# Kernel tuning notes

Hardware: AMD Instinct MI355X
Metric: run time of the kernel (lower is better)

## Reference

```python
import jax, jax.numpy as jnp
import numpy as np

B, N, D, DG = 32, 2048, 512, 1024


def layernorm(x, g, b, eps=1e-5):
    m = jnp.mean(x, axis=-1, keepdims=True)
    v = jnp.mean((x - m) ** 2, axis=-1, keepdims=True)
    return (x - m) * jax.lax.rsqrt(v + eps) * g + b


def simple_rms_norm(x, eps=1e-6):
    # parameter-free RMSNorm used inside Hgru1d
    return x * jax.lax.rsqrt(jnp.mean(x * x, axis=-1, keepdims=True) + eps)


def linear_recurrence(lam, u, reverse):
    # h_t = lam_t * h_{t-1} + u_t along axis=1, via associative scan
    def comb(c1, c2):
        a1, b1 = c1
        a2, b2 = c2
        return a1 * a2, a2 * b1 + b2
    return jax.lax.associative_scan(comb, (lam, u), axis=1, reverse=reverse)[1]


def hgru1d(x, lower_bound, Wi, bi, Wf, bf, Wg, bg, Wo, bo):
    # HGRN-style gated recurrence, bidirectional (causal=False, shared params)
    i = jax.nn.silu(x @ Wi + bi)                       # candidate input  [b,n,d]
    f = jax.nn.sigmoid(x @ Wf + bf)                    # forget gate      [b,n,d]
    lam = lower_bound + (1.0 - lower_bound) * f        # lower-bounded decay
    u = (1.0 - lam) * i
    h = linear_recurrence(lam, u, False) + linear_recurrence(lam, u, True)
    h = simple_rms_norm(h)
    g = jax.nn.sigmoid(x @ Wg + bg)                    # output gate
    return (h * g) @ Wo + bo


def glu(x, W1, b1, W2, b2, W3, b3):
    return (jax.nn.silu(x @ W1 + b1) * (x @ W2 + b2)) @ W3 + b3


def setup_inputs() -> dict:
    key = jax.random.key(0)
    ks = jax.random.split(key, 16)
    s = 0.02
    return {
        "x": jax.random.normal(ks[0], (B, N, D), dtype=jnp.float32),
        "lower_bound": 0,
        "Wi": jax.random.normal(ks[1], (D, D), jnp.float32) * s,
        "bi": jnp.zeros((D,), jnp.float32),
        "Wf": jax.random.normal(ks[2], (D, D), jnp.float32) * s,
        "bf": jnp.zeros((D,), jnp.float32),
        "Wg": jax.random.normal(ks[3], (D, D), jnp.float32) * s,
        "bg": jnp.zeros((D,), jnp.float32),
        "Wo": jax.random.normal(ks[4], (D, D), jnp.float32) * s,
        "bo": jnp.zeros((D,), jnp.float32),
        "tn_g": jnp.ones((D,), jnp.float32),
        "tn_b": jnp.zeros((D,), jnp.float32),
        "fn_g": jnp.ones((D,), jnp.float32),
        "fn_b": jnp.zeros((D,), jnp.float32),
        "W1": jax.random.normal(ks[5], (D, DG), jnp.float32) * s,
        "b1": jnp.zeros((DG,), jnp.float32),
        "W2": jax.random.normal(ks[6], (D, DG), jnp.float32) * s,
        "b2": jnp.zeros((DG,), jnp.float32),
        "W3": jax.random.normal(ks[7], (DG, D), jnp.float32) * s,
        "b3": jnp.zeros((D,), jnp.float32),
    }


def reference(x, lower_bound, Wi, bi, Wf, bf, Wg, bg, Wo, bo,
              tn_g, tn_b, fn_g, fn_b, W1, b1, W2, b2, W3, b3):
    lb = jnp.float32(lower_bound)
    # post-norm residual block
    x = x + layernorm(hgru1d(x, lb, Wi, bi, Wf, bf, Wg, bg, Wo, bo), tn_g, tn_b)
    x = x + layernorm(glu(x, W1, b1, W2, b2, W3, b3), fn_g, fn_b)
    return x
```

## Files before the change

kernel.cpp:

```cpp
#include <hip/hip_runtime.h>
#include <hip/hip_bf16.h>

#define BB 32
#define NN 2048
#define DD 512
#define DGG 1024
#define CC 32
#define LLEN 64

typedef short bf16x8 __attribute__((ext_vector_type(8)));
typedef float f32x4  __attribute__((ext_vector_type(4)));

__device__ __forceinline__ unsigned short f2bf(float f){
    __hip_bfloat16 h = __float2bfloat16(f);
    return *reinterpret_cast<unsigned short*>(&h);
}
__device__ __forceinline__ float bf2f(unsigned short u){
    unsigned int x = ((unsigned int)u) << 16;
    return __uint_as_float(x);
}
__device__ __forceinline__ float sigm(float x){ return 1.0f/(1.0f + __expf(-x)); }

__global__ __launch_bounds__(256)
void wt_prep(const float* __restrict__ in, unsigned short* __restrict__ out,
             int K, int N)
{
    __shared__ float t[32][33];
    const int tid = threadIdx.x;
    const int r = tid >> 3;
    const int c = (tid & 7) << 2;
    const int n0 = blockIdx.x * 32;
    const int k0 = blockIdx.y * 32;
    float4 v = *(const float4*)(in + (size_t)(k0 + r) * N + n0 + c);
    t[r][c] = v.x; t[r][c+1] = v.y; t[r][c+2] = v.z; t[r][c+3] = v.w;
    __syncthreads();
    ushort4 o;
    o.x = f2bf(t[c+0][r]); o.y = f2bf(t[c+1][r]);
    o.z = f2bf(t[c+2][r]); o.w = f2bf(t[c+3][r]);
    *(ushort4*)(out + (size_t)(n0 + r) * K + k0 + c) = o;
}

template<int MODE, int NB, bool ABF16>
__global__ __launch_bounds__(256)
void gemm_kernel(const void* __restrict__ Ap,
                 const unsigned short* __restrict__ Bt0,
                 const unsigned short* __restrict__ Bt1,
                 const unsigned short* __restrict__ Bt2,
                 const float* __restrict__ bias0, const float* __restrict__ bias1,
                 const float* __restrict__ bias2,
                 unsigned short* __restrict__ out0, unsigned short* __restrict__ out1,
                 unsigned short* __restrict__ out2,
                 const int* __restrict__ lbp, int K, int Nn)
{
    __shared__ unsigned short As[64][40];
    __shared__ unsigned short Bs[NB][64][40];

    const int tid  = threadIdx.x;
    const int m0   = blockIdx.y * 64;
    const int n0   = blockIdx.x * 64;
    const int lane = tid & 63;
    const int wave = tid >> 6;
    const int wr   = (wave >> 1) * 32;
    const int wc   = (wave & 1) * 32;
    const int lm   = lane & 15;
    const int quad = lane >> 4;

    f32x4 acc[NB][2][2];
    const f32x4 zero = {0.f, 0.f, 0.f, 0.f};
    #pragma unroll
    for (int a = 0; a < NB; ++a)
        for (int i = 0; i < 2; ++i)
            for (int j = 0; j < 2; ++j) acc[a][i][j] = zero;

    const float* Af = (const float*)Ap;
    const unsigned short* Ab = (const unsigned short*)Ap;
    const unsigned short* Bmats[3] = {Bt0, Bt1, Bt2};

    const int srow = tid >> 2;
    const int sc8  = (tid & 3) << 3;

    for (int k0 = 0; k0 < K; k0 += 32) {
        if (!ABF16) {
            #pragma unroll
            for (int it = 0; it < 2; ++it) {
                int cidx = tid + it * 256;
                int row  = cidx >> 3;
                int c4   = (cidx & 7) << 2;
                float4 v = *(const float4*)(Af + (size_t)(m0 + row) * K + k0 + c4);
                ushort4 o;
                o.x = f2bf(v.x); o.y = f2bf(v.y); o.z = f2bf(v.z); o.w = f2bf(v.w);
                *(ushort4*)&As[row][c4] = o;
            }
        } else {
            bf16x8 v = *(const bf16x8*)(Ab + (size_t)(m0 + srow) * K + k0 + sc8);
            *(bf16x8*)&As[srow][sc8] = v;
        }
        #pragma unroll
        for (int mat = 0; mat < NB; ++mat) {
            bf16x8 v = *(const bf16x8*)(Bmats[mat] + (size_t)(n0 + srow) * K + k0 + sc8);
            *(bf16x8*)&Bs[mat][srow][sc8] = v;
        }
        __syncthreads();

        bf16x8 a0 = *(const bf16x8*)&As[wr + lm][quad * 8];
        bf16x8 a1 = *(const bf16x8*)&As[wr + 16 + lm][quad * 8];
        #pragma unroll
        for (int mat = 0; mat < NB; ++mat) {
            #pragma unroll
            for (int ni = 0; ni < 2; ++ni) {
                bf16x8 b = *(const bf16x8*)&Bs[mat][wc + ni * 16 + lm][quad * 8];
                acc[mat][0][ni] = __builtin_amdgcn_mfma_f32_16x16x32_bf16(a0, b, acc[mat][0][ni], 0, 0, 0);
                acc[mat][1][ni] = __builtin_amdgcn_mfma_f32_16x16x32_bf16(a1, b, acc[mat][1][ni], 0, 0, 0);
            }
        }
        __syncthreads();
    }

    float lbv = 0.f;
    if constexpr (MODE == 1) lbv = (float)(*lbp);

    #pragma unroll
    for (int mi = 0; mi < 2; ++mi) {
        #pragma unroll
        for (int ni = 0; ni < 2; ++ni) {
            #pragma unroll
            for (int r = 0; r < 4; ++r) {
                int row = m0 + wr + mi * 16 + quad * 4 + r;
                int col = n0 + wc + ni * 16 + lm;
                size_t oidx = (size_t)row * Nn + col;
                if constexpr (MODE == 0) {
                    out0[oidx] = f2bf(acc[0][mi][ni][r] + bias0[col]);
                } else if constexpr (MODE == 1) {
                    float iv = acc[0][mi][ni][r] + bias0[col]; iv = iv * sigm(iv);
                    float fv = sigm(acc[1][mi][ni][r] + bias1[col]);
                    float gv = sigm(acc[2][mi][ni][r] + bias2[col]);
                    float lamv = lbv + (1.f - lbv) * fv;
                    float uv = (1.f - lamv) * iv;
                    out0[oidx] = f2bf(lamv);
                    out1[oidx] = f2bf(uv);
                    out2[oidx] = f2bf(gv);
                } else {
                    float s = acc[0][mi][ni][r] + bias0[col]; s = s * sigm(s);
                    float t = acc[1][mi][ni][r] + bias1[col];
                    out0[oidx] = f2bf(s * t);
                }
            }
        }
    }
}

__global__ __launch_bounds__(512)
void scan_agg(const unsigned short* __restrict__ lam, const unsigned short* __restrict__ u,
              float* __restrict__ Aarr, float* __restrict__ Vf, float* __restrict__ Vr)
{
    int bc = blockIdx.x;
    int b = bc >> 5, c = bc & 31;
    int d = threadIdx.x;
    size_t base = ((size_t)b * NN + c * LLEN) * DD + d;
    float A = 1.f, vf = 0.f, vr = 0.f;
    for (int t = 0; t < LLEN; ++t) {
        float lv = bf2f(lam[base + (size_t)t * DD]);
        float uv = bf2f(u[base + (size_t)t * DD]);
        vf = lv * vf + uv;
        vr += uv * A;
        A *= lv;
    }
    size_t o = (size_t)bc * DD + d;
    Aarr[o] = A; Vf[o] = vf; Vr[o] = vr;
}

__global__ __launch_bounds__(256)
void scan_comb(const float* __restrict__ Aarr, const float* __restrict__ Vf,
               const float* __restrict__ Vr, float* __restrict__ cf, float* __restrict__ cr)
{
    int g = blockIdx.x * 256 + threadIdx.x;
    int b = g >> 9, d = g & 511;
    float S = 0.f;
    for (int c = 0; c < CC; ++c) {
        size_t o = (size_t)(b * CC + c) * DD + d;
        cf[o] = S;
        S = Vf[o] + Aarr[o] * S;
    }
    S = 0.f;
    for (int c = CC - 1; c >= 0; --c) {
        size_t o = (size_t)(b * CC + c) * DD + d;
        cr[o] = S;
        S = Vr[o] + Aarr[o] * S;
    }
}

__global__ __launch_bounds__(256)
void scan_final(const unsigned short* __restrict__ lam, const unsigned short* __restrict__ u,
                const float* __restrict__ cf, const float* __restrict__ cr,
                float* __restrict__ h)
{
    int bid = blockIdx.x;
    int dh = bid & 1, c = (bid >> 1) & 31, b = bid >> 6;
    int d = dh * 256 + threadIdx.x;
    size_t base = ((size_t)b * NN + c * LLEN) * DD + d;
    size_t co   = (size_t)(b * CC + c) * DD + d;

    float hbuf[LLEN];
    float hf = cf[co];
    #pragma unroll
    for (int t = 0; t < LLEN; ++t) {
        float lv = bf2f(lam[base + (size_t)t * DD]);
        float uv = bf2f(u[base + (size_t)t * DD]);
        hf = lv * hf + uv;
        hbuf[t] = hf;
    }
    float hr = cr[co];
    #pragma unroll
    for (int t = LLEN - 1; t >= 0; --t) {
        float lv = bf2f(lam[base + (size_t)t * DD]);
        float uv = bf2f(u[base + (size_t)t * DD]);
        hr = lv * hr + uv;
        h[base + (size_t)t * DD] = hbuf[t] + hr;
    }
}

__global__ __launch_bounds__(256)
void rms_mul(const float* __restrict__ h, const unsigned short* __restrict__ g,
             unsigned short* __restrict__ hg)
{
    int row = blockIdx.x;
    size_t base = (size_t)row * DD;
    int tid = threadIdx.x, col = tid * 2;
    float2 v = *(const float2*)&h[base + col];
    float ss = v.x * v.x + v.y * v.y;
    #pragma unroll
    for (int off = 32; off > 0; off >>= 1) ss += __shfl_down(ss, off);
    __shared__ float ps[4];
    __shared__ float scale_s;
    if ((tid & 63) == 0) ps[tid >> 6] = ss;
    __syncthreads();
    if (tid == 0) scale_s = rsqrtf((ps[0] + ps[1] + ps[2] + ps[3]) * (1.f / DD) + 1e-6f);
    __syncthreads();
    float sc = scale_s;
    ushort2 gv = *(const ushort2*)&g[base + col];
    ushort2 o;
    o.x = f2bf(v.x * sc * bf2f(gv.x));
    o.y = f2bf(v.y * sc * bf2f(gv.y));
    *(ushort2*)&hg[base + col] = o;
}

__global__ __launch_bounds__(256)
void add_ln(const float* __restrict__ xin, const unsigned short* __restrict__ y,
            const float* __restrict__ gam, const float* __restrict__ bet,
            float* __restrict__ out)
{
    int row = blockIdx.x;
    size_t base = (size_t)row * DD;
    int tid = threadIdx.x, col = tid * 2;
    ushort2 yv = *(const ushort2*)&y[base + col];
    float vx = bf2f(yv.x), vy = bf2f(yv.y);
    float s = vx + vy;
    float ss = vx * vx + vy * vy;
    #pragma unroll
    for (int off = 32; off > 0; off >>= 1) {
        s  += __shfl_down(s, off);
        ss += __shfl_down(ss, off);
    }
    __shared__ float ps[8];
    __shared__ float stats[2];
    if ((tid & 63) == 0) { ps[tid >> 6] = s; ps[4 + (tid >> 6)] = ss; }
    __syncthreads();
    if (tid == 0) {
        float st  = ps[0] + ps[1] + ps[2] + ps[3];
        float sst = ps[4] + ps[5] + ps[6] + ps[7];
        float mean = st * (1.f / DD);
        float var  = sst * (1.f / DD) - mean * mean;
        stats[0] = mean; stats[1] = rsqrtf(var + 1e-5f);
    }
    __syncthreads();
    float mean = stats[0], inv = stats[1];
    float2 xv = *(const float2*)&xin[base + col];
    float2 gv = *(const float2*)&gam[col];
    float2 bv = *(const float2*)&bet[col];
    float2 o;
    o.x = xv.x + (vx - mean) * inv * gv.x + bv.x;
    o.y = xv.y + (vy - mean) * inv * gv.y + bv.y;
    *(float2*)&out[base + col] = o;
}

extern "C" void kernel_launch(void* const* d_in, const int* in_sizes, int n_in,
                              void* d_out, int out_size, void* d_ws, size_t ws_size,
                              hipStream_t stream)
{
    const float* x   = (const float*)d_in[0];
    const int*   lb  = (const int*)d_in[1];
    const float* Wi  = (const float*)d_in[2];
    const float* bi  = (const float*)d_in[3];
    const float* Wf  = (const float*)d_in[4];
    const float* bfp = (const float*)d_in[5];
    const float* Wg  = (const float*)d_in[6];
    const float* bg  = (const float*)d_in[7];
    const float* Wo  = (const float*)d_in[8];
    const float* bo  = (const float*)d_in[9];
    const float* tng = (const float*)d_in[10];
    const float* tnb = (const float*)d_in[11];
    const float* fng = (const float*)d_in[12];
    const float* fnb = (const float*)d_in[13];
    const float* W1  = (const float*)d_in[14];
    const float* b1  = (const float*)d_in[15];
    const float* W2  = (const float*)d_in[16];
    const float* b2  = (const float*)d_in[17];
    const float* W3  = (const float*)d_in[18];
    const float* b3  = (const float*)d_in[19];

    unsigned short* wbase = (unsigned short*)d_ws;
    unsigned short* WiT = wbase;
    unsigned short* WfT = WiT + 262144;
    unsigned short* WgT = WfT + 262144;
    unsigned short* WoT = WgT + 262144;
    unsigned short* W1T = WoT + 262144;
    unsigned short* W2T = W1T + 524288;
    unsigned short* W3T = W2T + 524288;
    const size_t WTOT = 4 * 262144 + 3 * 524288;

    wt_prep<<<dim3(16, 16), 256, 0, stream>>>(Wi, WiT, 512, 512);
    wt_prep<<<dim3(16, 16), 256, 0, stream>>>(Wf, WfT, 512, 512);
    wt_prep<<<dim3(16, 16), 256, 0, stream>>>(Wg, WgT, 512, 512);
    wt_prep<<<dim3(16, 16), 256, 0, stream>>>(Wo, WoT, 512, 512);
    wt_prep<<<dim3(32, 16), 256, 0, stream>>>(W1, W1T, 512, 1024);
    wt_prep<<<dim3(32, 16), 256, 0, stream>>>(W2, W2T, 512, 1024);
    wt_prep<<<dim3(16, 32), 256, 0, stream>>>(W3, W3T, 1024, 512);

    const size_t perB = (size_t)3 * NN * DD * 2 + (size_t)5 * CC * DD * 4;
    int Bch = 32;
    while (Bch > 1 && WTOT * 2 + (size_t)Bch * perB > ws_size) Bch >>= 1;
    const int nch = BB / Bch;

    const size_t slabE = (size_t)Bch * NN * DD;

    for (int ch = 0; ch < nch; ++ch) {
        const size_t r0 = (size_t)ch * Bch * NN;
        const float* xc = x + r0 * DD;
        unsigned short* S0 = wbase + WTOT;
        unsigned short* S1 = S0 + slabE;
        unsigned short* S2 = S0 + 2 * slabE;
        float* small = (float*)(S0 + 3 * slabE);
        const size_t agg = (size_t)Bch * CC * DD;
        float* Aarr = small;
        float* VfP  = small + agg;
        float* VrP  = small + 2 * agg;
        float* cfP  = small + 3 * agg;
        float* crP  = small + 4 * agg;
        float* hout = (float*)d_out + r0 * DD;

        gemm_kernel<1, 3, false><<<dim3(DD / 64, Bch * NN / 64), 256, 0, stream>>>(
            xc, WiT, WfT, WgT, bi, bfp, bg, S0, S1, S2, lb, DD, DD);
        scan_agg<<<Bch * CC, 512, 0, stream>>>(S0, S1, Aarr, VfP, VrP);
        scan_comb<<<(Bch * DD) / 256, 256, 0, stream>>>(Aarr, VfP, VrP, cfP, crP);
        scan_final<<<Bch * CC * 2, 256, 0, stream>>>(S0, S1, cfP, crP, hout);
        rms_mul<<<Bch * NN, 256, 0, stream>>>(hout, S2, S2);
        gemm_kernel<0, 1, true><<<dim3(DD / 64, Bch * NN / 64), 256, 0, stream>>>(
            S2, WoT, nullptr, nullptr, bo, nullptr, nullptr, S0, nullptr, nullptr,
            nullptr, DD, DD);
        add_ln<<<Bch * NN, 256, 0, stream>>>(xc, S0, tng, tnb, hout);
        gemm_kernel<2, 2, false><<<dim3(DGG / 64, Bch * NN / 64), 256, 0, stream>>>(
            hout, W1T, W2T, nullptr, b1, b2, nullptr, S0, nullptr, nullptr, nullptr, DD, DGG);
        gemm_kernel<0, 1, true><<<dim3(DD / 64, Bch * NN / 64), 256, 0, stream>>>(
            S0, W3T, nullptr, nullptr, b3, nullptr, nullptr, S2, nullptr, nullptr,
            nullptr, DGG, DD);
        add_ln<<<Bch * NN, 256, 0, stream>>>(hout, S2, fng, fnb, hout);
    }
}
```

Before: 1.380 ms.

## Use 128x128 direct-to-LDS bf16 GEMM tiles and split fused multi-weight GEMMs

Replaces the 64x64 multi-matrix GEMM with a single-weight 128x128-tile GEMM that loads bf16 tiles into LDS via global_load_lds, giving each wave a 64x64 sub-tile with 16 MFMAs per k-step. Activations are pre-cast to bf16 by a new cast kernel, and add_ln also writes a bf16 copy so the GLU GEMMs read bf16 inputs. The fused three-gate and two-gate GEMMs are split into separate launches that pass intermediates through a staged buffer. The goal is more operand reuse per LDS load and less in-loop conversion, at the cost of extra launches, extra intermediate traffic and a larger workspace. The main loop still has no double buffering, and it is left uncertain whether direct LDS loads without padding cause bank conflicts.

```diff
diff --git a/kernel.cpp b/kernel.cpp
--- a/kernel.cpp
+++ b/kernel.cpp
@@ -20,6 +20,12 @@
     return __uint_as_float(x);
 }
 __device__ __forceinline__ float sigm(float x){ return 1.0f/(1.0f + __expf(-x)); }
+
+__device__ __forceinline__ void gl_lds16(const unsigned short* g, unsigned short* l){
+    __builtin_amdgcn_global_load_lds(
+        (const __attribute__((address_space(1))) unsigned int*)g,
+        (__attribute__((address_space(3))) unsigned int*)l, 16, 0, 0);
+}
 
 __global__ __launch_bounds__(256)
 void wt_prep(const float* __restrict__ in, unsigned short* __restrict__ out,
@@ -40,109 +46,105 @@
     *(ushort4*)(out + (size_t)(n0 + r) * K + k0 + c) = o;
 }
 
-template<int MODE, int NB, bool ABF16>
-__global__ __launch_bounds__(256)
-void gemm_kernel(const void* __restrict__ Ap,
-                 const unsigned short* __restrict__ Bt0,
-                 const unsigned short* __restrict__ Bt1,
-                 const unsigned short* __restrict__ Bt2,
-                 const float* __restrict__ bias0, const float* __restrict__ bias1,
-                 const float* __restrict__ bias2,
-                 unsigned short* __restrict__ out0, unsigned short* __restrict__ out1,
-                 unsigned short* __restrict__ out2,
-                 const int* __restrict__ lbp, int K, int Nn)
-{
-    __shared__ unsigned short As[64][40];
-    __shared__ unsigned short Bs[NB][64][40];
+__global__ __launch_bounds__(256)
+void cast_bf16(const float* __restrict__ in, unsigned short* __restrict__ out)
+{
+    size_t i = ((size_t)blockIdx.x * 256 + threadIdx.x) * 4;
+    float4 v = *(const float4*)(in + i);
+    ushort4 o;
+    o.x = f2bf(v.x); o.y = f2bf(v.y); o.z = f2bf(v.z); o.w = f2bf(v.w);
+    *(ushort4*)(out + i) = o;
+}
+
+template<int MODE>
+__global__ __launch_bounds__(256)
+void gemm128(const unsigned short* __restrict__ A,
+             const unsigned short* __restrict__ Bt,
+             const float* __restrict__ bias,
+             const unsigned short* __restrict__ staged,
+             unsigned short* __restrict__ out0,
+             unsigned short* __restrict__ out1,
+             const int* __restrict__ lbp, int K, int Nn)
+{
+    __shared__ unsigned short As[128 * 32];
+    __shared__ unsigned short Bs[128 * 32];
 
     const int tid  = threadIdx.x;
-    const int m0   = blockIdx.y * 64;
-    const int n0   = blockIdx.x * 64;
+    const int wave = tid >> 6;
     const int lane = tid & 63;
-    const int wave = tid >> 6;
-    const int wr   = (wave >> 1) * 32;
-    const int wc   = (wave & 1) * 32;
+    const int m0   = blockIdx.y * 128;
+    const int n0   = blockIdx.x * 128;
+    const int wr   = (wave >> 1) * 64;
+    const int wc   = (wave & 1) * 64;
     const int lm   = lane & 15;
     const int quad = lane >> 4;
 
-    f32x4 acc[NB][2][2];
+    f32x4 acc[4][4];
     const f32x4 zero = {0.f, 0.f, 0.f, 0.f};
     #pragma unroll
-    for (int a = 0; a < NB; ++a)
-        for (int i = 0; i < 2; ++i)
-            for (int j = 0; j < 2; ++j) acc[a][i][j] = zero;
-
-    const float* Af = (const float*)Ap;
-    const unsigned short* Ab = (const unsigned short*)Ap;
-    const unsigned short* Bmats[3] = {Bt0, Bt1, Bt2};
-
-    const int srow = tid >> 2;
-    const int sc8  = (tid & 3) << 3;
+    for (int i = 0; i < 4; ++i)
+        for (int j = 0; j < 4; ++j) acc[i][j] = zero;
+
+    const int srow = wave * 32 + (lane >> 2);
+    const int skof = (lane & 3) << 3;
+    const unsigned short* ga0 = A  + (size_t)(m0 + srow) * K + skof;
+    const unsigned short* ga1 = ga0 + (size_t)16 * K;
+    const unsigned short* gb0 = Bt + (size_t)(n0 + srow) * K + skof;
+    const unsigned short* gb1 = gb0 + (size_t)16 * K;
+    unsigned short* la0 = &As[(wave * 32) * 32];
+    unsigned short* la1 = &As[(wave * 32 + 16) * 32];
+    unsigned short* lb0 = &Bs[(wave * 32) * 32];
+    unsigned short* lb1 = &Bs[(wave * 32 + 16) * 32];
 
     for (int k0 = 0; k0 < K; k0 += 32) {
-        if (!ABF16) {
+        gl_lds16(ga0, la0); gl_lds16(ga1, la1);
+        gl_lds16(gb0, lb0); gl_lds16(gb1, lb1);
+        ga0 += 32; ga1 += 32; gb0 += 32; gb1 += 32;
+        __syncthreads();
+
+        bf16x8 a[4], b[4];
+        #pragma unroll
+        for (int mi = 0; mi < 4; ++mi)
+            a[mi] = *(const bf16x8*)&As[(wr + mi * 16 + lm) * 32 + quad * 8];
+        #pragma unroll
+        for (int ni = 0; ni < 4; ++ni)
+            b[ni] = *(const bf16x8*)&Bs[(wc + ni * 16 + lm) * 32 + quad * 8];
+        #pragma unroll
+        for (int mi = 0; mi < 4; ++mi)
             #pragma unroll
-            for (int it = 0; it < 2; ++it) {
-                int cidx = tid + it * 256;
-                int row  = cidx >> 3;
-                int c4   = (cidx & 7) << 2;
-                float4 v = *(const float4*)(Af + (size_t)(m0 + row) * K + k0 + c4);
-                ushort4 o;
-                o.x = f2bf(v.x); o.y = f2bf(v.y); o.z = f2bf(v.z); o.w = f2bf(v.w);
-                *(ushort4*)&As[row][c4] = o;
-            }
-        } else {
-            bf16x8 v = *(const bf16x8*)(Ab + (size_t)(m0 + srow) * K + k0 + sc8);
-            *(bf16x8*)&As[srow][sc8] = v;
-        }
+            for (int ni = 0; ni < 4; ++ni)
+                acc[mi][ni] = __builtin_amdgcn_mfma_f32_16x16x32_bf16(a[mi], b[ni], acc[mi][ni], 0, 0, 0);
+        __syncthreads();
+    }
+
+    float lbv = 0.f;
+    if constexpr (MODE == 3) lbv = (float)(*lbp);
+
+    #pragma unroll
+    for (int mi = 0; mi < 4; ++mi) {
         #pragma unroll
-        for (int mat = 0; mat < NB; ++mat) {
-            bf16x8 v = *(const bf16x8*)(Bmats[mat] + (size_t)(n0 + srow) * K + k0 + sc8);
-            *(bf16x8*)&Bs[mat][srow][sc8] = v;
-        }
-        __syncthreads();
-
-        bf16x8 a0 = *(const bf16x8*)&As[wr + lm][quad * 8];
-        bf16x8 a1 = *(const bf16x8*)&As[wr + 16 + lm][quad * 8];
-        #pragma unroll
-        for (int mat = 0; mat < NB; ++mat) {
-            #pragma unroll
-            for (int ni = 0; ni < 2; ++ni) {
-                bf16x8 b = *(const bf16x8*)&Bs[mat][wc + ni * 16 + lm][quad * 8];
-                acc[mat][0][ni] = __builtin_amdgcn_mfma_f32_16x16x32_bf16(a0, b, acc[mat][0][ni], 0, 0, 0);
-                acc[mat][1][ni] = __builtin_amdgcn_mfma_f32_16x16x32_bf16(a1, b, acc[mat][1][ni], 0, 0, 0);
-            }
-        }
-        __syncthreads();
-    }
-
-    float lbv = 0.f;
-    if constexpr (MODE == 1) lbv = (float)(*lbp);
-
-    #pragma unroll
-    for (int mi = 0; mi < 2; ++mi) {
-        #pragma unroll
-        for (int ni = 0; ni < 2; ++ni) {
+        for (int ni = 0; ni < 4; ++ni) {
+            int col = n0 + wc + ni * 16 + lm;
+            float bcol = bias[col];
             #pragma unroll
             for (int r = 0; r < 4; ++r) {
                 int row = m0 + wr + mi * 16 + quad * 4 + r;
-                int col = n0 + wc + ni * 16 + lm;
                 size_t oidx = (size_t)row * Nn + col;
+                float v = acc[mi][ni][r] + bcol;
                 if constexpr (MODE == 0) {
-                    out0[oidx] = f2bf(acc[0][mi][ni][r] + bias0[col]);
+                    out0[oidx] = f2bf(v);
                 } else if constexpr (MODE == 1) {
-                    float iv = acc[0][mi][ni][r] + bias0[col]; iv = iv * sigm(iv);
-                    float fv = sigm(acc[1][mi][ni][r] + bias1[col]);
-                    float gv = sigm(acc[2][mi][ni][r] + bias2[col]);
+                    out0[oidx] = f2bf(v * sigm(v));
+                } else if constexpr (MODE == 2) {
+                    out0[oidx] = f2bf(sigm(v));
+                } else if constexpr (MODE == 3) {
+                    float fv = sigm(v);
                     float lamv = lbv + (1.f - lbv) * fv;
-                    float uv = (1.f - lamv) * iv;
+                    float si = bf2f(staged[oidx]);
                     out0[oidx] = f2bf(lamv);
-                    out1[oidx] = f2bf(uv);
-                    out2[oidx] = f2bf(gv);
+                    out1[oidx] = f2bf((1.f - lamv) * si);
                 } else {
-                    float s = acc[0][mi][ni][r] + bias0[col]; s = s * sigm(s);
-                    float t = acc[1][mi][ni][r] + bias1[col];
-                    out0[oidx] = f2bf(s * t);
+                    out0[oidx] = f2bf(bf2f(staged[oidx]) * v);
                 }
             }
         }
@@ -247,7 +249,7 @@
 __global__ __launch_bounds__(256)
 void add_ln(const float* __restrict__ xin, const unsigned short* __restrict__ y,
             const float* __restrict__ gam, const float* __restrict__ bet,
-            float* __restrict__ out)
+            float* __restrict__ out, unsigned short* __restrict__ outb)
 {
     int row = blockIdx.x;
     size_t base = (size_t)row * DD;
@@ -281,6 +283,10 @@
     o.x = xv.x + (vx - mean) * inv * gv.x + bv.x;
     o.y = xv.y + (vy - mean) * inv * gv.y + bv.y;
     *(float2*)&out[base + col] = o;
+    if (outb) {
+        ushort2 ob; ob.x = f2bf(o.x); ob.y = f2bf(o.y);
+        *(ushort2*)&outb[base + col] = ob;
+    }
 }
 
 extern "C" void kernel_launch(void* const* d_in, const int* in_sizes, int n_in,
@@ -326,7 +332,7 @@
     wt_prep<<<dim3(32, 16), 256, 0, stream>>>(W2, W2T, 512, 1024);
     wt_prep<<<dim3(16, 32), 256, 0, stream>>>(W3, W3T, 1024, 512);
 
-    const size_t perB = (size_t)3 * NN * DD * 2 + (size_t)5 * CC * DD * 4;
+    const size_t perB = (size_t)4 * NN * DD * 2 + (size_t)5 * CC * DD * 4;
     int Bch = 32;
     while (Bch > 1 && WTOT * 2 + (size_t)Bch * perB > ws_size) Bch >>= 1;
     const int nch = BB / Bch;
@@ -335,11 +341,13 @@
 
     for (int ch = 0; ch < nch; ++ch) {
         const size_t r0 = (size_t)ch * Bch * NN;
+        const int Mc = Bch * NN;
         const float* xc = x + r0 * DD;
         unsigned short* S0 = wbase + WTOT;
         unsigned short* S1 = S0 + slabE;
         unsigned short* S2 = S0 + 2 * slabE;
-        float* small = (float*)(S0 + 3 * slabE);
+        unsigned short* S3 = S0 + 3 * slabE;
+        float* small = (float*)(S0 + 4 * slabE);
         const size_t agg = (size_t)Bch * CC * DD;
         float* Aarr = small;
         float* VfP  = small + agg;
@@ -348,21 +356,26 @@
         float* crP  = small + 4 * agg;
         float* hout = (float*)d_out + r0 * DD;
 
-        gemm_kernel<1, 3, false><<<dim3(DD / 64, Bch * NN / 64), 256, 0, stream>>>(
-            xc, WiT, WfT, WgT, bi, bfp, bg, S0, S1, S2, lb, DD, DD);
-        scan_agg<<<Bch * CC, 512, 0, stream>>>(S0, S1, Aarr, VfP, VrP);
+        cast_bf16<<<Mc / 2, 256, 0, stream>>>(xc, S3);
+        gemm128<1><<<dim3(DD / 128, Mc / 128), 256, 0, stream>>>(
+            S3, WiT, bi, nullptr, S0, nullptr, nullptr, DD, DD);
+        gemm128<3><<<dim3(DD / 128, Mc / 128), 256, 0, stream>>>(
+            S3, WfT, bfp, S0, S1, S0, lb, DD, DD);
+        gemm128<2><<<dim3(DD / 128, Mc / 128), 256, 0, stream>>>(
+            S3, WgT, bg, nullptr, S2, nullptr, nullptr, DD, DD);
+        scan_agg<<<Bch * CC, 512, 0, stream>>>(S1, S0, Aarr, VfP, VrP);
         scan_comb<<<(Bch * DD) / 256, 256, 0, stream>>>(Aarr, VfP, VrP, cfP, crP);
-        scan_final<<<Bch * CC * 2, 256, 0, stream>>>(S0, S1, cfP, crP, hout);
-        rms_mul<<<Bch * NN, 256, 0, stream>>>(hout, S2, S2);
-        gemm_kernel<0, 1, true><<<dim3(DD / 64, Bch * NN / 64), 256, 0, stream>>>(
-            S2, WoT, nullptr, nullptr, bo, nullptr, nullptr, S0, nullptr, nullptr,
-            nullptr, DD, DD);
-        add_ln<<<Bch * NN, 256, 0, stream>>>(xc, S0, tng, tnb, hout);
-        gemm_kernel<2, 2, false><<<dim3(DGG / 64, Bch * NN / 64), 256, 0, stream>>>(
-            hout, W1T, W2T, nullptr, b1, b2, nullptr, S0, nullptr, nullptr, nullptr, DD, DGG);
-        gemm_kernel<0, 1, true><<<dim3(DD / 64, Bch * NN / 64), 256, 0, stream>>>(
-            S0, W3T, nullptr, nullptr, b3, nullptr, nullptr, S2, nullptr, nullptr,
-            nullptr, DGG, DD);
-        add_ln<<<Bch * NN, 256, 0, stream>>>(hout, S2, fng, fnb, hout);
-    }
-}
+        scan_final<<<Bch * CC * 2, 256, 0, stream>>>(S1, S0, cfP, crP, hout);
+        rms_mul<<<Mc, 256, 0, stream>>>(hout, S2, S2);
+        gemm128<0><<<dim3(DD / 128, Mc / 128), 256, 0, stream>>>(
+            S2, WoT, bo, nullptr, S0, nullptr, nullptr, DD, DD);
+        add_ln<<<Mc, 256, 0, stream>>>(xc, S0, tng, tnb, hout, S3);
+        gemm128<1><<<dim3(DGG / 128, Mc / 128), 256, 0, stream>>>(
+            S3, W1T, b1, nullptr, S1, nullptr, nullptr, DD, DGG);
+        gemm128<4><<<dim3(DGG / 128, Mc / 128), 256, 0, stream>>>(
+            S3, W2T, b2, S1, S1, nullptr, nullptr, DD, DGG);
+        gemm128<0><<<dim3(DD / 128, Mc / 128), 256, 0, stream>>>(
+            S1, W3T, b3, nullptr, S0, nullptr, nullptr, DGG, DD);
+        add_ln<<<Mc, 256, 0, stream>>>(hout, S0, fng, fnb, hout, nullptr);
+    }
+}
```

After: 1.291 ms. -6.4%, faster.
